# Optimization experiments

Measured on AMD Instinct MI355X. Metric: run time of the kernel, lower is better.

Reference implementation:

```python
import math
import jax, jax.numpy as jnp
import numpy as np

B, S, C = 2, 1024, 1024   # batch, seq, d_model
H, D = 16, 64             # heads, head_dim
R = 16                    # num_rules
RK = 32                   # shared_rank = round(sqrt(min(in,out)))
FA = 32                   # Kronecker factors: 1024 = 32*32 -> a=b=c=d=32
ROPE_BASE = 10000.0


def setup_inputs() -> dict:
    key = jax.random.key(0)
    ks = jax.random.split(key, 8)
    inv_c = 1.0 / math.sqrt(C)
    return {
        "x": jax.random.normal(ks[0], (B, S, C), jnp.float32),
        "shared_in": jax.random.normal(ks[1], (4, C, RK), jnp.float32) * inv_c,
        "shared_out": jax.random.normal(ks[2], (4, RK, C), jnp.float32) * (1.0 / math.sqrt(RK)),
        "rule_U": jax.random.normal(ks[3], (4, R, FA, FA), jnp.float32) * (1.0 / FA),  # kron_std=1/sqrt(a*b)
        "rule_V": jax.random.normal(ks[4], (4, R, FA, FA), jnp.float32) * (1.0 / FA),
        "rule_gain": jnp.full((4, R), 1.0 / math.sqrt(R), jnp.float32),
        "wq": jax.random.normal(ks[5], (C, C), jnp.float32) * inv_c,
        "wkv": jax.random.normal(ks[6], (C, 2 * C), jnp.float32) * inv_c,
        "gate": jnp.full((C,), 0.01, jnp.float32),
        "rule_ids": jax.random.randint(ks[7], (B, S), 0, R),
    }


def _rule_proj(xf, rid, si, so, ru, rv, g):
    # Same math as the sorted/grouped/padded torch dispatch, per-token gather form.
    base = (xf @ si) @ so                              # [N, C]
    N = xf.shape[0]
    c, a = ru.shape[-2], ru.shape[-1]
    d, b = rv.shape[-2], rv.shape[-1]
    xm = xf.reshape(N, b, a)
    xu = jnp.einsum('nba,nca->nbc', xm, ru[rid])       # (b,a)@(a,c)
    vxu = jnp.einsum('ndb,nbc->ndc', rv[rid], xu)      # (d,b)@(b,c)
    return base + vxu.reshape(N, d * c) * g[rid][:, None]


def _rope(q, k):
    seq, hd = q.shape[2], q.shape[3]
    pos = jnp.arange(seq, dtype=jnp.float32)[:, None]
    div = jnp.exp(jnp.arange(0, hd, 2, dtype=jnp.float32) * (-math.log(ROPE_BASE) / hd))
    f = pos * div                                      # [S, hd/2]
    sin, cos = jnp.sin(f), jnp.cos(f)

    def rot(t):
        t1, t2 = t[..., 0::2], t[..., 1::2]
        return jnp.stack([t1 * cos - t2 * sin, t2 * cos + t1 * sin], axis=-1).reshape(t.shape)

    return rot(q), rot(k)


def _hier(x, rule_ids, wq, wkv, gate):
    # Causal per-rule running-mean memory, queried over the U (=R) rule axis.
    k_val, v_val = jnp.split(x @ wkv, 2, axis=-1)
    q_val = x @ wq
    m = jax.nn.one_hot(rule_ids, R, dtype=x.dtype)     # [B,S,U]
    k_sum = jnp.cumsum(jnp.einsum('bsu,bsc->bsuc', m, k_val), axis=1)
    v_sum = jnp.cumsum(jnp.einsum('bsu,bsc->bsuc', m, v_val), axis=1)
    count = jnp.maximum(jnp.cumsum(m, axis=1), 1.0)[..., None]
    k_mean = k_sum / count
    v_mean = v_sum / count
    logits = jnp.einsum('bsc,bsuc->bsu', q_val, k_mean) * (1.0 / math.sqrt(C))
    w = jax.nn.softmax(logits, axis=-1)
    return jnp.einsum('bsu,bsuc->bsc', w, v_mean) * gate


def reference(x, shared_in, shared_out, rule_U, rule_V, rule_gain, wq, wkv, gate, rule_ids):
    Bx, Sx, Cx = x.shape
    xf = x.reshape(-1, Cx)
    rid = rule_ids.reshape(-1)
    q = _rule_proj(xf, rid, shared_in[0], shared_out[0], rule_U[0], rule_V[0], rule_gain[0])
    k = _rule_proj(xf, rid, shared_in[1], shared_out[1], rule_U[1], rule_V[1], rule_gain[1])
    v = _rule_proj(xf, rid, shared_in[2], shared_out[2], rule_U[2], rule_V[2], rule_gain[2])

    def heads(t):
        return t.reshape(Bx, Sx, H, D).transpose(0, 2, 1, 3)  # [B,H,S,D]

    q, k, v = heads(q), heads(k), heads(v)
    q, k = _rope(q, k)
    scores = jnp.einsum('bhqd,bhkd->bhqk', q, k) * (1.0 / math.sqrt(D))
    causal = jnp.tril(jnp.ones((Sx, Sx), dtype=bool))
    scores = jnp.where(causal, scores, jnp.finfo(scores.dtype).min)
    attn = jax.nn.softmax(scores, axis=-1)
    ctx = jnp.einsum('bhqk,bhkd->bhqd', attn, v)
    ctx = ctx.transpose(0, 2, 1, 3).reshape(Bx * Sx, Cx)
    out = _rule_proj(ctx, rid, shared_in[3], shared_out[3], rule_U[3], rule_V[3], rule_gain[3])
    out = out.reshape(Bx, Sx, Cx)
    return out + _hier(x, rule_ids, wq, wkv, gate)
```

## Files before the change

### kernel.cpp

```cpp
#include <hip/hip_runtime.h>

#define B_ 2
#define S_ 1024
#define C_ 1024
#define H_ 16
#define D_ 64
#define R_ 16
#define RK_ 32
#define FA_ 32
#define N_ (B_*S_)
#define NCH_ 16

__global__ __launch_bounds__(256) void gemm_k(const float* __restrict__ A,
                                              const float* __restrict__ W,
                                              float* __restrict__ Co,
                                              int M, int K, int Nn)
{
    __shared__ float As[16][132];
    __shared__ float Ws[16][132];
    const int tid = threadIdx.x;
    const int tx = tid & 15, ty = tid >> 4;
    const int m0 = blockIdx.y << 7, n0 = blockIdx.x << 7;

    float acc[8][8] = {};
    const int ar = tid >> 1;
    const int ak = (tid & 1) << 3;
    const int wk = tid >> 4;
    const int wc = (tid & 15) << 3;

    const float* Ap = A + (m0 + ar)*K + ak;
    const float* Wp = W + wk*Nn + n0 + wc;

    for (int k0 = 0; k0 < K; k0 += 16) {
        float4 a0 = *reinterpret_cast<const float4*>(Ap + k0);
        float4 a1 = *reinterpret_cast<const float4*>(Ap + k0 + 4);
        float4 w0 = *reinterpret_cast<const float4*>(Wp + k0*Nn);
        float4 w1 = *reinterpret_cast<const float4*>(Wp + k0*Nn + 4);
        __syncthreads();
        As[ak+0][ar] = a0.x; As[ak+1][ar] = a0.y;
        As[ak+2][ar] = a0.z; As[ak+3][ar] = a0.w;
        As[ak+4][ar] = a1.x; As[ak+5][ar] = a1.y;
        As[ak+6][ar] = a1.z; As[ak+7][ar] = a1.w;
        *reinterpret_cast<float4*>(&Ws[wk][wc])     = w0;
        *reinterpret_cast<float4*>(&Ws[wk][wc + 4]) = w1;
        __syncthreads();
        #pragma unroll
        for (int kk = 0; kk < 16; ++kk) {
            float a[8], b[8];
            *reinterpret_cast<float4*>(&a[0]) = *reinterpret_cast<const float4*>(&As[kk][ty<<3]);
            *reinterpret_cast<float4*>(&a[4]) = *reinterpret_cast<const float4*>(&As[kk][(ty<<3)+4]);
            *reinterpret_cast<float4*>(&b[0]) = *reinterpret_cast<const float4*>(&Ws[kk][tx<<3]);
            *reinterpret_cast<float4*>(&b[4]) = *reinterpret_cast<const float4*>(&Ws[kk][(tx<<3)+4]);
            #pragma unroll
            for (int i = 0; i < 8; ++i)
                #pragma unroll
                for (int j = 0; j < 8; ++j)
                    acc[i][j] += a[i]*b[j];
        }
    }
    #pragma unroll
    for (int i = 0; i < 8; ++i) {
        float* cp = Co + (m0 + (ty<<3) + i)*Nn + n0 + (tx<<3);
        *reinterpret_cast<float4*>(cp)     = make_float4(acc[i][0], acc[i][1], acc[i][2], acc[i][3]);
        *reinterpret_cast<float4*>(cp + 4) = make_float4(acc[i][4], acc[i][5], acc[i][6], acc[i][7]);
    }
}

__global__ __launch_bounds__(256) void proj_k(const float* __restrict__ xin,
                                              const float* __restrict__ si,
                                              const float* __restrict__ so,
                                              const float* __restrict__ ru,
                                              const float* __restrict__ rv,
                                              const float* __restrict__ gain,
                                              const int* __restrict__ rids,
                                              float* __restrict__ outp,
                                              int mode)
{
    __shared__ float xrow[C_];
    __shared__ float tpart[8][RK_];
    __shared__ float tvec[RK_];
    __shared__ float rut[FA_*33];
    __shared__ float rvs[FA_*FA_];
    __shared__ float xu[FA_*FA_];
    __shared__ float obuf[C_];
    const int tid = threadIdx.x;
    const int n = blockIdx.x;
    const int rid = rids[n];
    const float g = gain[rid];

    *reinterpret_cast<float4*>(&xrow[tid<<2]) =
        *reinterpret_cast<const float4*>(xin + n*C_ + (tid<<2));
    #pragma unroll
    for (int q = 0; q < 4; ++q) {
        int idx = tid + (q<<8);
        rut[(idx & 31)*33 + (idx >> 5)] = ru[rid*1024 + idx];
        rvs[idx] = rv[rid*1024 + idx];
    }
    __syncthreads();
    {
        const int col = tid & 31, sl = tid >> 5;
        const int i0 = sl << 7;
        float a = 0.f;
        for (int i = 0; i < 128; ++i)
            a += xrow[i0 + i] * si[(i0 + i)*RK_ + col];
        tpart[sl][col] = a;
    }
    __syncthreads();
    if (tid < 32) {
        float a = 0.f;
        #pragma unroll
        for (int sl = 0; sl < 8; ++sl) a += tpart[sl][tid];
        tvec[tid] = a;
    }
    __syncthreads();
    #pragma unroll
    for (int q = 0; q < 4; ++q) {
        int idx = tid + (q<<8);
        int bb = idx >> 5, cc = idx & 31;
        float a = 0.f;
        #pragma unroll 8
        for (int aa = 0; aa < 32; ++aa)
            a += xrow[(bb<<5) + aa] * rut[aa*33 + cc];
        xu[idx] = a;
    }
    __syncthreads();
    #pragma unroll
    for (int q = 0; q < 4; ++q) {
        int m = tid + (q<<8);
        int dd = m >> 5, cc = m & 31;
        float ab = 0.f;
        #pragma unroll 8
        for (int j = 0; j < RK_; ++j)
            ab += tvec[j] * so[j*C_ + m];
        float av = 0.f;
        #pragma unroll 8
        for (int bb = 0; bb < 32; ++bb)
            av += rvs[(dd<<5) + bb] * xu[(bb<<5) + cc];
        obuf[m] = ab + av * g;
    }
    __syncthreads();
    if (mode == 1) {
        const float pos = (float)(n & (S_-1));
        #pragma unroll
        for (int q = 0; q < 2; ++q) {
            int pi = tid + (q<<8);
            int ii = pi & 31;
            float f = pos * expf((float)(ii<<1) * -0.14391157f);
            float sn = sinf(f), cs = cosf(f);
            float e = obuf[pi<<1], o = obuf[(pi<<1)+1];
            outp[n*C_ + (pi<<1)]     = e*cs - o*sn;
            outp[n*C_ + (pi<<1) + 1] = o*cs + e*sn;
        }
    } else if (mode == 2) {
        #pragma unroll
        for (int q = 0; q < 4; ++q) {
            int m = tid + (q<<8);
            outp[n*C_ + m] += obuf[m];
        }
    } else {
        #pragma unroll
        for (int q = 0; q < 4; ++q) {
            int m = tid + (q<<8);
            outp[n*C_ + m] = obuf[m];
        }
    }
}

__global__ __launch_bounds__(256) void attn_k(const float* __restrict__ qb,
                                              const float* __restrict__ kb,
                                              const float* __restrict__ vb,
                                              float* __restrict__ ctx)
{
    __shared__ float Qs[64*68];
    __shared__ float KtPs[64*68];
    __shared__ float Vs[64*68];
    const int tid = threadIdx.x;
    const int tx = tid & 15, ty = tid >> 4;
    const int qt = blockIdx.x;
    const int b = blockIdx.y >> 4, h = blockIdx.y & 15;
    const float* qbase = qb + (b*S_)*C_ + h*64;
    const float* kbase = kb + (b*S_)*C_ + h*64;
    const float* vbase = vb + (b*S_)*C_ + h*64;

    #pragma unroll
    for (int q = 0; q < 4; ++q) {
        int idx = tid + (q<<8);
        int r = idx >> 4, d4 = (idx & 15) << 2;
        *reinterpret_cast<float4*>(&Qs[r*68 + d4]) =
            *reinterpret_cast<const float4*>(qbase + (qt*64 + r)*C_ + d4);
    }
    float acc[4][4] = {};
    float mrun[4] = {-3e38f, -3e38f, -3e38f, -3e38f};
    float lrun[4] = {};
    const int row0 = qt*64 + (ty<<2);

    for (int kt = 0; kt <= qt; ++kt) {
        __syncthreads();
        #pragma unroll
        for (int q = 0; q < 4; ++q) {
            int idx = tid + (q<<8);
            int r = idx >> 4, d4 = (idx & 15) << 2;
            float4 kv = *reinterpret_cast<const float4*>(kbase + (kt*64 + r)*C_ + d4);
            KtPs[(d4+0)*68 + r] = kv.x;
            KtPs[(d4+1)*68 + r] = kv.y;
            KtPs[(d4+2)*68 + r] = kv.z;
            KtPs[(d4+3)*68 + r] = kv.w;
            *reinterpret_cast<float4*>(&Vs[r*68 + d4]) =
                *reinterpret_cast<const float4*>(vbase + (kt*64 + r)*C_ + d4);
        }
        __syncthreads();
        float s[4][4] = {};
        #pragma unroll 4
        for (int d0 = 0; d0 < 64; d0 += 4) {
            float4 q4[4], k4[4];
            #pragma unroll
            for (int i = 0; i < 4; ++i)
                q4[i] = *reinterpret_cast<const float4*>(&Qs[((ty<<2)+i)*68 + d0]);
            #pragma unroll
            for (int u = 0; u < 4; ++u)
                k4[u] = *reinterpret_cast<const float4*>(&KtPs[(d0+u)*68 + (tx<<2)]);
            #pragma unroll
            for (int i = 0; i < 4; ++i) {
                float qa[4] = {q4[i].x, q4[i].y, q4[i].z, q4[i].w};
                #pragma unroll
                for (int u = 0; u < 4; ++u) {
                    s[i][0] += qa[u]*k4[u].x;
                    s[i][1] += qa[u]*k4[u].y;
                    s[i][2] += qa[u]*k4[u].z;
                    s[i][3] += qa[u]*k4[u].w;
                }
            }
        }
        __syncthreads();
        const int col0 = kt*64 + (tx<<2);
        #pragma unroll
        for (int i = 0; i < 4; ++i) {
            #pragma unroll
            for (int j = 0; j < 4; ++j) {
                float sv = s[i][j]*0.125f;
                if (col0 + j > row0 + i) sv = -3e38f;
                s[i][j] = sv;
            }
            float mx = fmaxf(fmaxf(s[i][0], s[i][1]), fmaxf(s[i][2], s[i][3]));
            #pragma unroll
            for (int off = 1; off < 16; off <<= 1)
                mx = fmaxf(mx, __shfl_xor(mx, off, 64));
            float mnew = fmaxf(mrun[i], mx);
            float corr = expf(mrun[i] - mnew);
            float rs = 0.f;
            #pragma unroll
            for (int j = 0; j < 4; ++j) {
                float p = expf(s[i][j] - mnew);
                s[i][j] = p;
                rs += p;
            }
            #pragma unroll
            for (int off = 1; off < 16; off <<= 1)
                rs += __shfl_xor(rs, off, 64);
            mrun[i] = mnew;
            lrun[i] = lrun[i]*corr + rs;
            acc[i][0] *= corr; acc[i][1] *= corr; acc[i][2] *= corr; acc[i][3] *= corr;
            *reinterpret_cast<float4*>(&KtPs[((ty<<2)+i)*68 + (tx<<2)]) =
                make_float4(s[i][0], s[i][1], s[i][2], s[i][3]);
        }
        __syncthreads();
        #pragma unroll 4
        for (int k0 = 0; k0 < 64; k0 += 4) {
            float4 p4[4], v4[4];
            #pragma unroll
            for (int i = 0; i < 4; ++i)
                p4[i] = *reinterpret_cast<const float4*>(&KtPs[((ty<<2)+i)*68 + k0]);
            #pragma unroll
            for (int u = 0; u < 4; ++u)
                v4[u] = *reinterpret_cast<const float4*>(&Vs[(k0+u)*68 + (tx<<2)]);
            #pragma unroll
            for (int i = 0; i < 4; ++i) {
                float pa[4] = {p4[i].x, p4[i].y, p4[i].z, p4[i].w};
                #pragma unroll
                for (int u = 0; u < 4; ++u) {
                    acc[i][0] += pa[u]*v4[u].x;
                    acc[i][1] += pa[u]*v4[u].y;
                    acc[i][2] += pa[u]*v4[u].z;
                    acc[i][3] += pa[u]*v4[u].w;
                }
            }
        }
    }
    #pragma unroll
    for (int i = 0; i < 4; ++i) {
        float inv = 1.f / lrun[i];
        *reinterpret_cast<float4*>(ctx + (b*S_ + qt*64 + (ty<<2) + i)*C_ + h*64 + (tx<<2)) =
            make_float4(acc[i][0]*inv, acc[i][1]*inv, acc[i][2]*inv, acc[i][3]*inv);
    }
}

__global__ __launch_bounds__(256) void hchunk_k(const float* __restrict__ kvb,
                                                const int* __restrict__ rids,
                                                float* __restrict__ chk,
                                                float* __restrict__ chv)
{
    __shared__ float ks[R_*256];
    __shared__ float vs[R_*256];
    const int tid = threadIdx.x;
    const int cs = blockIdx.x, ch = blockIdx.y, b = blockIdx.z;
    const int c = (cs<<8) + tid;
    #pragma unroll
    for (int u = 0; u < R_; ++u) { ks[(u<<8) + tid] = 0.f; vs[(u<<8) + tid] = 0.f; }
    const int* rp = rids + b*S_ + (ch<<6);
    const float* kvp = kvb + (b*S_ + (ch<<6))*2048 + c;
    for (int s2 = 0; s2 < 64; ++s2) {
        const int u = rp[s2];
        ks[(u<<8) + tid] += kvp[0];
        vs[(u<<8) + tid] += kvp[1024];
        kvp += 2048;
    }
    #pragma unroll
    for (int u = 0; u < R_; ++u) {
        chk[((b*NCH_ + ch)*R_ + u)*C_ + c] = ks[(u<<8) + tid];
        chv[((b*NCH_ + ch)*R_ + u)*C_ + c] = vs[(u<<8) + tid];
    }
}

__global__ __launch_bounds__(256) void hscan_k(float* __restrict__ chk,
                                               float* __restrict__ chv)
{
    const int idx = blockIdx.x*256 + threadIdx.x;
    const int b = idx >> 14;
    const int rc = idx & 16383;
    const int base = b*(NCH_*R_*C_) + rc;
    float rk = 0.f, rv2 = 0.f;
    for (int ch = 0; ch < NCH_; ++ch) {
        const int o = base + ch*(R_*C_);
        float tk = chk[o]; chk[o] = rk; rk += tk;
        float tv = chv[o]; chv[o] = rv2; rv2 += tv;
    }
}

__global__ __launch_bounds__(512) void hweights_k(const float* __restrict__ chk,
                                                  const float* __restrict__ kvb,
                                                  const float* __restrict__ qv,
                                                  const int* __restrict__ rids,
                                                  float* __restrict__ lgp)
{
    __shared__ float ksum[R_*512];
    __shared__ int cnt[R_];
    const int tid = threadIdx.x;
    const int half = blockIdx.x, ch = blockIdx.y, b = blockIdx.z;
    const int c0 = half << 9;
    #pragma unroll
    for (int u = 0; u < R_; ++u)
        ksum[(u<<9) + tid] = chk[((b*NCH_ + ch)*R_ + u)*C_ + c0 + tid];
    if (tid < R_) cnt[tid] = 0;
    __syncthreads();
    for (int t = tid; t < ch*64; t += 512)
        atomicAdd(&cnt[rids[b*S_ + t]], 1);
    __syncthreads();
    const int wv = tid >> 6, ln = tid & 63;
    for (int s = 0; s < 64; ++s) {
        const int row = b*S_ + (ch<<6) + s;
        const int u = rids[row];
        ksum[(u<<9) + tid] += kvb[row*2048 + c0 + tid];
        if (tid == 0) cnt[u] += 1;
        __syncthreads();
        #pragma unroll
        for (int uu = 0; uu < 2; ++uu) {
            const int ur = (wv<<1) + uu;
            float part = 0.f;
            #pragma unroll
            for (int j = 0; j < 8; ++j) {
                int c = ln + (j<<6);
                part += qv[row*C_ + c0 + c] * ksum[(ur<<9) + c];
            }
            #pragma unroll
            for (int off = 1; off < 64; off <<= 1)
                part += __shfl_xor(part, off, 64);
            if (ln == 0)
                lgp[(row<<5) + (ur<<1) + half] =
                    part * 0.03125f / (float)(cnt[ur] > 0 ? cnt[ur] : 1);
        }
        __syncthreads();
    }
}

__global__ __launch_bounds__(256) void wfinal_k(const float* __restrict__ lgp,
                                                float* __restrict__ wout)
{
    const int row = blockIdx.x*256 + threadIdx.x;
    float lg[R_];
    float mx = -3e38f;
    #pragma unroll
    for (int u = 0; u < R_; ++u) {
        lg[u] = lgp[(row<<5) + (u<<1)] + lgp[(row<<5) + (u<<1) + 1];
        mx = fmaxf(mx, lg[u]);
    }
    float sm = 0.f;
    #pragma unroll
    for (int u = 0; u < R_; ++u) { lg[u] = expf(lg[u] - mx); sm += lg[u]; }
    const float inv = 1.f / sm;
    #pragma unroll
    for (int u = 0; u < R_; ++u)
        wout[(row<<4) + u] = lg[u] * inv;
}

__global__ __launch_bounds__(512) void hmix_k(const float* __restrict__ chv,
                                              const float* __restrict__ kvb,
                                              const int* __restrict__ rids,
                                              const float* __restrict__ wout,
                                              const float* __restrict__ gate,
                                              float* __restrict__ outp)
{
    __shared__ float vsum[R_*512];
    __shared__ int cnt[R_];
    __shared__ float rcq[R_];
    __shared__ float wsh[R_];
    const int tid = threadIdx.x;
    const int half = blockIdx.x, ch = blockIdx.y, b = blockIdx.z;
    const int c0 = half << 9;
    #pragma unroll
    for (int u = 0; u < R_; ++u)
        vsum[(u<<9) + tid] = chv[((b*NCH_ + ch)*R_ + u)*C_ + c0 + tid];
    if (tid < R_) cnt[tid] = 0;
    __syncthreads();
    for (int t = tid; t < ch*64; t += 512)
        atomicAdd(&cnt[rids[b*S_ + t]], 1);
    const float gt = gate[c0 + tid];
    __syncthreads();
    for (int s = 0; s < 64; ++s) {
        const int row = b*S_ + (ch<<6) + s;
        const int u = rids[row];
        vsum[(u<<9) + tid] += kvb[row*2048 + 1024 + c0 + tid];
        if (tid == 0) cnt[u] += 1;
        __syncthreads();
        if (tid < R_) {
            rcq[tid] = 1.f / (float)(cnt[tid] > 0 ? cnt[tid] : 1);
            wsh[tid] = wout[(row<<4) + tid];
        }
        __syncthreads();
        float a = 0.f;
        #pragma unroll
        for (int u2 = 0; u2 < R_; ++u2)
            a += wsh[u2] * rcq[u2] * vsum[(u2<<9) + tid];
        outp[row*C_ + c0 + tid] = a * gt;
        __syncthreads();
    }
}

extern "C" void kernel_launch(void* const* d_in, const int* in_sizes, int n_in,
                              void* d_out, int out_size, void* d_ws, size_t ws_size,
                              hipStream_t stream) {
    (void)in_sizes; (void)n_in; (void)out_size; (void)ws_size;
    const float* x    = (const float*)d_in[0];
    const float* sin_ = (const float*)d_in[1];
    const float* sout = (const float*)d_in[2];
    const float* rU   = (const float*)d_in[3];
    const float* rV   = (const float*)d_in[4];
    const float* rG   = (const float*)d_in[5];
    const float* wq   = (const float*)d_in[6];
    const float* wkv  = (const float*)d_in[7];
    const float* gate = (const float*)d_in[8];
    const int*   rids = (const int*)d_in[9];
    float* out = (float*)d_out;
    float* ws  = (float*)d_ws;

    float* QV   = ws;
    float* KV   = ws + 2097152;
    float* CHK  = ws + 6291456;
    float* CHV  = ws + 6815744;
    float* WOUT = ws + 7340032;
    float* LGP  = ws + 7372800;
    float* qb   = ws;
    float* kb   = ws + 2097152;
    float* vbuf = ws + 4194304;
    float* ctxb = ws + 6291456;

    gemm_k<<<dim3(8,  16), 256, 0, stream>>>(x, wq,  QV, N_, C_, C_);
    gemm_k<<<dim3(16, 16), 256, 0, stream>>>(x, wkv, KV, N_, C_, 2*C_);
    hchunk_k<<<dim3(4, NCH_, B_), 256, 0, stream>>>(KV, rids, CHK, CHV);
    hscan_k<<<dim3(128), 256, 0, stream>>>(CHK, CHV);
    hweights_k<<<dim3(2, NCH_, B_), 512, 0, stream>>>(CHK, KV, QV, rids, LGP);
    wfinal_k<<<dim3(8), 256, 0, stream>>>(LGP, WOUT);
    hmix_k<<<dim3(2, NCH_, B_), 512, 0, stream>>>(CHV, KV, rids, WOUT, gate, out);

    proj_k<<<dim3(N_), 256, 0, stream>>>(x, sin_,       sout,       rU,       rV,       rG,    rids, qb,   1);
    proj_k<<<dim3(N_), 256, 0, stream>>>(x, sin_+32768, sout+32768, rU+16384, rV+16384, rG+16, rids, kb,   1);
    proj_k<<<dim3(N_), 256, 0, stream>>>(x, sin_+65536, sout+65536, rU+32768, rV+32768, rG+32, rids, vbuf, 0);

    attn_k<<<dim3(16, 32), 256, 0, stream>>>(qb, kb, vbuf, ctxb);

    proj_k<<<dim3(N_), 256, 0, stream>>>(ctxb, sin_+98304, sout+98304, rU+49152, rV+49152, rG+48, rids, out, 2);
}
```

Baseline: 787.5 us.

## Rewrite causal attention kernel with bf16 MFMA for QK^T and PV

Replaces the fp32 scalar-FMA flash attention with a wave-level design using 16x16x32 bf16 MFMA instructions. Q is held in registers as bf16 fragments, K and a transposed V are converted to bf16 in shared memory, and the softmax probabilities are written per wave as bf16 before the PV product. The aim is to move attention compute onto the matrix cores and halve LDS traffic. The trade-off is lower precision for Q, K, V and P, plus 16-bit transposed LDS stores for V that may cause bank conflicts.

```diff
diff --git a/kernel.cpp b/kernel.cpp
--- a/kernel.cpp
+++ b/kernel.cpp
@@ -10,6 +10,18 @@
 #define FA_ 32
 #define N_ (B_*S_)
 #define NCH_ 16
+
+typedef __attribute__((ext_vector_type(8))) short bf16x8;
+typedef __attribute__((ext_vector_type(4))) float f32x4;
+#define MFMA_BF16(A,B,C) __builtin_amdgcn_mfma_f32_16x16x32_bf16(A,B,C,0,0,0)
+
+__device__ inline unsigned short f2bf(float x) {
+    unsigned u = __float_as_uint(x);
+    return (unsigned short)((u + 0x7FFFu + ((u >> 16) & 1u)) >> 16);
+}
+__device__ inline unsigned pack2(float a, float b) {
+    return (unsigned)f2bf(a) | ((unsigned)f2bf(b) << 16);
+}
 
 __global__ __launch_bounds__(256) void gemm_k(const float* __restrict__ A,
                                               const float* __restrict__ W,
@@ -171,126 +183,158 @@
                                               const float* __restrict__ vb,
                                               float* __restrict__ ctx)
 {
-    __shared__ float Qs[64*68];
-    __shared__ float KtPs[64*68];
-    __shared__ float Vs[64*68];
+    __shared__ unsigned short Ks[64*72];
+    __shared__ unsigned short Vt[64*72];
+    __shared__ unsigned short Ps[64*72];
     const int tid = threadIdx.x;
-    const int tx = tid & 15, ty = tid >> 4;
+    const int lane = tid & 63, w = tid >> 6;
+    const int lm = lane & 15, lg = lane >> 4;
     const int qt = blockIdx.x;
     const int b = blockIdx.y >> 4, h = blockIdx.y & 15;
-    const float* qbase = qb + (b*S_)*C_ + h*64;
-    const float* kbase = kb + (b*S_)*C_ + h*64;
-    const float* vbase = vb + (b*S_)*C_ + h*64;
-
-    #pragma unroll
-    for (int q = 0; q < 4; ++q) {
-        int idx = tid + (q<<8);
-        int r = idx >> 4, d4 = (idx & 15) << 2;
-        *reinterpret_cast<float4*>(&Qs[r*68 + d4]) =
-            *reinterpret_cast<const float4*>(qbase + (qt*64 + r)*C_ + d4);
-    }
-    float acc[4][4] = {};
-    float mrun[4] = {-3e38f, -3e38f, -3e38f, -3e38f};
-    float lrun[4] = {};
-    const int row0 = qt*64 + (ty<<2);
+    const float* qbase = qb + (size_t)(b*S_)*C_ + h*64;
+    const float* kbase = kb + (size_t)(b*S_)*C_ + h*64;
+    const float* vbase = vb + (size_t)(b*S_)*C_ + h*64;
+
+    bf16x8 qf[2];
+    {
+        const int qrow = qt*64 + w*16 + lm;
+        #pragma unroll
+        for (int kd = 0; kd < 2; ++kd) {
+            const float* qp = qbase + (size_t)qrow*C_ + kd*32 + lg*8;
+            float4 f0 = *reinterpret_cast<const float4*>(qp);
+            float4 f1 = *reinterpret_cast<const float4*>(qp + 4);
+            unsigned u0 = pack2(f0.x, f0.y), u1 = pack2(f0.z, f0.w);
+            unsigned u2 = pack2(f1.x, f1.y), u3 = pack2(f1.z, f1.w);
+            bf16x8 t;
+            t[0] = (short)(u0 & 0xFFFF); t[1] = (short)(u0 >> 16);
+            t[2] = (short)(u1 & 0xFFFF); t[3] = (short)(u1 >> 16);
+            t[4] = (short)(u2 & 0xFFFF); t[5] = (short)(u2 >> 16);
+            t[6] = (short)(u3 & 0xFFFF); t[7] = (short)(u3 >> 16);
+            qf[kd] = t;
+        }
+    }
+
+    f32x4 oacc0 = {0.f,0.f,0.f,0.f}, oacc1 = {0.f,0.f,0.f,0.f};
+    f32x4 oacc2 = {0.f,0.f,0.f,0.f}, oacc3 = {0.f,0.f,0.f,0.f};
+    float mrun[4] = {-3e38f,-3e38f,-3e38f,-3e38f};
+    float lrun[4] = {0.f,0.f,0.f,0.f};
+
+    const int skey = tid >> 2, sd = (tid & 3) << 4;
+    const int vkey = lane,     vd = w << 4;
 
     for (int kt = 0; kt <= qt; ++kt) {
         __syncthreads();
-        #pragma unroll
-        for (int q = 0; q < 4; ++q) {
-            int idx = tid + (q<<8);
-            int r = idx >> 4, d4 = (idx & 15) << 2;
-            float4 kv = *reinterpret_cast<const float4*>(kbase + (kt*64 + r)*C_ + d4);
-            KtPs[(d4+0)*68 + r] = kv.x;
-            KtPs[(d4+1)*68 + r] = kv.y;
-            KtPs[(d4+2)*68 + r] = kv.z;
-            KtPs[(d4+3)*68 + r] = kv.w;
-            *reinterpret_cast<float4*>(&Vs[r*68 + d4]) =
-                *reinterpret_cast<const float4*>(vbase + (kt*64 + r)*C_ + d4);
-        }
-        __syncthreads();
-        float s[4][4] = {};
-        #pragma unroll 4
-        for (int d0 = 0; d0 < 64; d0 += 4) {
-            float4 q4[4], k4[4];
-            #pragma unroll
-            for (int i = 0; i < 4; ++i)
-                q4[i] = *reinterpret_cast<const float4*>(&Qs[((ty<<2)+i)*68 + d0]);
-            #pragma unroll
-            for (int u = 0; u < 4; ++u)
-                k4[u] = *reinterpret_cast<const float4*>(&KtPs[(d0+u)*68 + (tx<<2)]);
-            #pragma unroll
-            for (int i = 0; i < 4; ++i) {
-                float qa[4] = {q4[i].x, q4[i].y, q4[i].z, q4[i].w};
-                #pragma unroll
-                for (int u = 0; u < 4; ++u) {
-                    s[i][0] += qa[u]*k4[u].x;
-                    s[i][1] += qa[u]*k4[u].y;
-                    s[i][2] += qa[u]*k4[u].z;
-                    s[i][3] += qa[u]*k4[u].w;
-                }
+        {
+            const float* kp = kbase + (size_t)(kt*64 + skey)*C_ + sd;
+            float4 k0 = *reinterpret_cast<const float4*>(kp);
+            float4 k1 = *reinterpret_cast<const float4*>(kp + 4);
+            float4 k2 = *reinterpret_cast<const float4*>(kp + 8);
+            float4 k3 = *reinterpret_cast<const float4*>(kp + 12);
+            uint4 p0 = { pack2(k0.x,k0.y), pack2(k0.z,k0.w), pack2(k1.x,k1.y), pack2(k1.z,k1.w) };
+            uint4 p1 = { pack2(k2.x,k2.y), pack2(k2.z,k2.w), pack2(k3.x,k3.y), pack2(k3.z,k3.w) };
+            *reinterpret_cast<uint4*>(&Ks[skey*72 + sd])     = p0;
+            *reinterpret_cast<uint4*>(&Ks[skey*72 + sd + 8]) = p1;
+        }
+        {
+            const float* vp = vbase + (size_t)(kt*64 + vkey)*C_ + vd;
+            float4 v0 = *reinterpret_cast<const float4*>(vp);
+            float4 v1 = *reinterpret_cast<const float4*>(vp + 4);
+            float4 v2 = *reinterpret_cast<const float4*>(vp + 8);
+            float4 v3 = *reinterpret_cast<const float4*>(vp + 12);
+            float vv[16] = {v0.x,v0.y,v0.z,v0.w, v1.x,v1.y,v1.z,v1.w,
+                            v2.x,v2.y,v2.z,v2.w, v3.x,v3.y,v3.z,v3.w};
+            #pragma unroll
+            for (int j = 0; j < 16; ++j)
+                Vt[(vd + j)*72 + vkey] = f2bf(vv[j]);
+        }
+        __syncthreads();
+
+        f32x4 sa[4];
+        #pragma unroll
+        for (int T = 0; T < 4; ++T) {
+            f32x4 z = {0.f,0.f,0.f,0.f};
+            #pragma unroll
+            for (int kd = 0; kd < 2; ++kd) {
+                bf16x8 kf = *reinterpret_cast<const bf16x8*>(&Ks[(T*16 + lm)*72 + kd*32 + lg*8]);
+                z = MFMA_BF16(qf[kd], kf, z);
             }
-        }
-        __syncthreads();
-        const int col0 = kt*64 + (tx<<2);
-        #pragma unroll
-        for (int i = 0; i < 4; ++i) {
-            #pragma unroll
-            for (int j = 0; j < 4; ++j) {
-                float sv = s[i][j]*0.125f;
-                if (col0 + j > row0 + i) sv = -3e38f;
-                s[i][j] = sv;
+            sa[T] = z;
+        }
+
+        const bool diag = (kt == qt);
+        float sv[4][4], pv[4][4];
+        #pragma unroll
+        for (int T = 0; T < 4; ++T)
+            #pragma unroll
+            for (int r = 0; r < 4; ++r) {
+                float val = sa[T][r] * 0.125f;
+                if (diag && (T*16 + lm > w*16 + lg*4 + r)) val = -3e38f;
+                sv[T][r] = val;
             }
-            float mx = fmaxf(fmaxf(s[i][0], s[i][1]), fmaxf(s[i][2], s[i][3]));
-            #pragma unroll
-            for (int off = 1; off < 16; off <<= 1)
-                mx = fmaxf(mx, __shfl_xor(mx, off, 64));
-            float mnew = fmaxf(mrun[i], mx);
-            float corr = expf(mrun[i] - mnew);
+        #pragma unroll
+        for (int r = 0; r < 4; ++r) {
+            float mrow = fmaxf(fmaxf(sv[0][r], sv[1][r]), fmaxf(sv[2][r], sv[3][r]));
+            mrow = fmaxf(mrow, __shfl_xor(mrow, 1, 64));
+            mrow = fmaxf(mrow, __shfl_xor(mrow, 2, 64));
+            mrow = fmaxf(mrow, __shfl_xor(mrow, 4, 64));
+            mrow = fmaxf(mrow, __shfl_xor(mrow, 8, 64));
+            float mnew = fmaxf(mrun[r], mrow);
+            float corr = expf(mrun[r] - mnew);
             float rs = 0.f;
             #pragma unroll
-            for (int j = 0; j < 4; ++j) {
-                float p = expf(s[i][j] - mnew);
-                s[i][j] = p;
+            for (int T = 0; T < 4; ++T) {
+                float p = expf(sv[T][r] - mnew);
+                pv[T][r] = p;
                 rs += p;
             }
-            #pragma unroll
-            for (int off = 1; off < 16; off <<= 1)
-                rs += __shfl_xor(rs, off, 64);
-            mrun[i] = mnew;
-            lrun[i] = lrun[i]*corr + rs;
-            acc[i][0] *= corr; acc[i][1] *= corr; acc[i][2] *= corr; acc[i][3] *= corr;
-            *reinterpret_cast<float4*>(&KtPs[((ty<<2)+i)*68 + (tx<<2)]) =
-                make_float4(s[i][0], s[i][1], s[i][2], s[i][3]);
-        }
-        __syncthreads();
-        #pragma unroll 4
-        for (int k0 = 0; k0 < 64; k0 += 4) {
-            float4 p4[4], v4[4];
-            #pragma unroll
-            for (int i = 0; i < 4; ++i)
-                p4[i] = *reinterpret_cast<const float4*>(&KtPs[((ty<<2)+i)*68 + k0]);
-            #pragma unroll
-            for (int u = 0; u < 4; ++u)
-                v4[u] = *reinterpret_cast<const float4*>(&Vs[(k0+u)*68 + (tx<<2)]);
-            #pragma unroll
-            for (int i = 0; i < 4; ++i) {
-                float pa[4] = {p4[i].x, p4[i].y, p4[i].z, p4[i].w};
-                #pragma unroll
-                for (int u = 0; u < 4; ++u) {
-                    acc[i][0] += pa[u]*v4[u].x;
-                    acc[i][1] += pa[u]*v4[u].y;
-                    acc[i][2] += pa[u]*v4[u].z;
-                    acc[i][3] += pa[u]*v4[u].w;
-                }
-            }
-        }
-    }
-    #pragma unroll
-    for (int i = 0; i < 4; ++i) {
-        float inv = 1.f / lrun[i];
-        *reinterpret_cast<float4*>(ctx + (b*S_ + qt*64 + (ty<<2) + i)*C_ + h*64 + (tx<<2)) =
-            make_float4(acc[i][0]*inv, acc[i][1]*inv, acc[i][2]*inv, acc[i][3]*inv);
+            rs += __shfl_xor(rs, 1, 64);
+            rs += __shfl_xor(rs, 2, 64);
+            rs += __shfl_xor(rs, 4, 64);
+            rs += __shfl_xor(rs, 8, 64);
+            mrun[r] = mnew;
+            lrun[r] = lrun[r]*corr + rs;
+            oacc0[r] *= corr; oacc1[r] *= corr; oacc2[r] *= corr; oacc3[r] *= corr;
+        }
+
+        #pragma unroll
+        for (int T = 0; T < 4; ++T)
+            #pragma unroll
+            for (int r = 0; r < 4; ++r)
+                Ps[(w*16 + lg*4 + r)*72 + T*16 + lm] = f2bf(pv[T][r]);
+        asm volatile("s_waitcnt lgkmcnt(0)" ::: "memory");
+        __builtin_amdgcn_sched_barrier(0);
+
+        bf16x8 pf0 = *reinterpret_cast<const bf16x8*>(&Ps[(w*16 + lm)*72 + 0*32 + lg*8]);
+        bf16x8 pf1 = *reinterpret_cast<const bf16x8*>(&Ps[(w*16 + lm)*72 + 1*32 + lg*8]);
+        {
+            bf16x8 vf;
+            vf = *reinterpret_cast<const bf16x8*>(&Vt[(0*16 + lm)*72 + 0*32 + lg*8]);
+            oacc0 = MFMA_BF16(pf0, vf, oacc0);
+            vf = *reinterpret_cast<const bf16x8*>(&Vt[(0*16 + lm)*72 + 1*32 + lg*8]);
+            oacc0 = MFMA_BF16(pf1, vf, oacc0);
+            vf = *reinterpret_cast<const bf16x8*>(&Vt[(1*16 + lm)*72 + 0*32 + lg*8]);
+            oacc1 = MFMA_BF16(pf0, vf, oacc1);
+            vf = *reinterpret_cast<const bf16x8*>(&Vt[(1*16 + lm)*72 + 1*32 + lg*8]);
+            oacc1 = MFMA_BF16(pf1, vf, oacc1);
+            vf = *reinterpret_cast<const bf16x8*>(&Vt[(2*16 + lm)*72 + 0*32 + lg*8]);
+            oacc2 = MFMA_BF16(pf0, vf, oacc2);
+            vf = *reinterpret_cast<const bf16x8*>(&Vt[(2*16 + lm)*72 + 1*32 + lg*8]);
+            oacc2 = MFMA_BF16(pf1, vf, oacc2);
+            vf = *reinterpret_cast<const bf16x8*>(&Vt[(3*16 + lm)*72 + 0*32 + lg*8]);
+            oacc3 = MFMA_BF16(pf0, vf, oacc3);
+            vf = *reinterpret_cast<const bf16x8*>(&Vt[(3*16 + lm)*72 + 1*32 + lg*8]);
+            oacc3 = MFMA_BF16(pf1, vf, oacc3);
+        }
+    }
+
+    #pragma unroll
+    for (int r = 0; r < 4; ++r) {
+        float inv = 1.f / lrun[r];
+        float* cp = ctx + (size_t)(b*S_ + qt*64 + w*16 + lg*4 + r)*C_ + h*64;
+        cp[0*16 + lm] = oacc0[r]*inv;
+        cp[1*16 + lm] = oacc1[r]*inv;
+        cp[2*16 + lm] = oacc2[r]*inv;
+        cp[3*16 + lm] = oacc3[r]*inv;
     }
 }
 
```

New measurement: 686.6 us. 12.8% less time.
